# Optimization experiments

Hardware: AMD Instinct MI355X
Metric: run time of the kernel (lower is better)

Reference implementation:

```python
import jax, jax.numpy as jnp
import numpy as np

HS = 128  # hidden_size
B, L = 2, 1024


def setup_inputs() -> dict:
    key = jax.random.key(0)
    k = jax.random.split(key, 3)
    d = HS
    X = jax.random.normal(k[0], (B, L, d), dtype=jnp.float32)
    # mlp: Linear(4d -> d), GELU, Linear(d -> 1)
    W1 = jax.random.normal(k[1], (4 * d, d), dtype=jnp.float32) / np.sqrt(4 * d).astype(np.float32)
    b1 = jnp.zeros((d,), dtype=jnp.float32)
    W2 = jax.random.normal(k[2], (d, 1), dtype=jnp.float32) / np.sqrt(d).astype(np.float32)
    b2 = jnp.zeros((1,), dtype=jnp.float32)
    return {"X": X, "W1": W1, "b1": b1, "W2": W2, "b2": b2}


def reference(X, W1, b1, W2, b2):
    # f = cat([Xi, Xj, Xi-Xj, Xi*Xj]) @ W1  decomposes exactly into four matmuls:
    #   Xi@(Wi+Wd) + Xj@(Wj-Wd) + (Xi*Xj)@Wp
    # avoiding the (b,l,l,4d) concat tensor.
    b, l, d = X.shape
    Wi, Wj, Wd, Wp = jnp.split(W1, 4, axis=0)  # each (d, h)
    A = X @ (Wi + Wd)                           # (b,l,h): depends on i only
    Bm = X @ (Wj - Wd)                          # (b,l,h): depends on j only
    P = jnp.einsum('bid,bjd,dh->bijh', X, X, Wp)  # elementwise-product term
    h = jax.nn.gelu(A[:, :, None, :] + Bm[:, None, :, :] + P + b1,
                    approximate=False)          # (b,l,l,h), exact GELU like nn.GELU()
    out = jnp.einsum('bijh,ho->bij', h, W2) + b2[0]  # (b,l,l)
    out = jax.nn.relu(out)
    out = 0.5 * (out + jnp.swapaxes(out, 1, 2))      # symmetrize
    diag_mask = 1.0 - jnp.eye(l, dtype=out.dtype)    # zero the diagonal
    return out * diag_mask
```

## Files before the change

### kernel.cpp

```cpp
#include <hip/hip_runtime.h>


typedef __attribute__((ext_vector_type(8))) short short8;
typedef __attribute__((ext_vector_type(16))) float f32x16;
typedef __attribute__((ext_vector_type(2))) float f32x2;

#define NT 32
#define NTRI 528
#define IPB 16

__device__ __forceinline__ unsigned short f2bf(float f) {
  unsigned int u = __float_as_uint(f);
  u = (u + 0x7fffu + ((u >> 16) & 1u)) >> 16;
  return (unsigned short)u;
}

__device__ __forceinline__ short8 pack8(float4 a, float4 b) {
  short8 r;
  r[0] = (short)f2bf(a.x); r[1] = (short)f2bf(a.y);
  r[2] = (short)f2bf(a.z); r[3] = (short)f2bf(a.w);
  r[4] = (short)f2bf(b.x); r[5] = (short)f2bf(b.y);
  r[6] = (short)f2bf(b.z); r[7] = (short)f2bf(b.w);
  return r;
}

__device__ __forceinline__ f32x2 gelu_2(f32x2 x) {
  f32x2 t = x * x;
  f32x2 u = x * __builtin_elementwise_fma(t, (f32x2)0.10295205f, (f32x2)2.30220725f);
  f32x2 e;
  e[0] = __builtin_amdgcn_exp2f(u[0]);
  e[1] = __builtin_amdgcn_exp2f(u[1]);
  f32x2 ep = e + 1.0f;
  f32x2 r;
  r[0] = __builtin_amdgcn_rcpf(ep[0]);
  r[1] = __builtin_amdgcn_rcpf(ep[1]);
  return __builtin_elementwise_fma(-x, r, x);
}

__global__ void k0_prep_w(const float* __restrict__ W1, unsigned short* __restrict__ wsT) {
  int idx = blockIdx.x * 256 + threadIdx.x;
  int arr = idx >> 14, rem = idx & 16383, h = rem >> 7, d = rem & 127;
  float v;
  if (arr == 0)      v = W1[d * 128 + h] + W1[(256 + d) * 128 + h];
  else if (arr == 1) v = W1[(128 + d) * 128 + h] - W1[(256 + d) * 128 + h];
  else               v = W1[(384 + d) * 128 + h];
  wsT[idx] = f2bf(v);
}

__global__ __launch_bounds__(256) void k1_ab(const float* __restrict__ X,
                                             const unsigned short* __restrict__ wsT,
                                             const float* __restrict__ b1,
                                             float* __restrict__ Aout,
                                             float* __restrict__ Bout) {
  int tid = threadIdx.x, w = tid >> 6, lane = tid & 63, jl = lane & 31, hi = lane >> 5;
  int row0 = blockIdx.x * 64;
  int c0 = w * 64;
  f32x16 a00 = (f32x16)0.f, a01 = (f32x16)0.f, a10 = (f32x16)0.f, a11 = (f32x16)0.f;
#pragma unroll
  for (int s = 0; s < 8; ++s) {
    const float* xp0 = X + (size_t)(row0 + jl) * 128 + s * 16 + hi * 8;
    const float* xp1 = xp0 + 32 * 128;
    short8 fa0 = pack8(*(const float4*)xp0, *(const float4*)(xp0 + 4));
    short8 fa1 = pack8(*(const float4*)xp1, *(const float4*)(xp1 + 4));
    short8 fb0 = *(const short8*)(wsT + (size_t)(c0 + jl) * 128 + s * 16 + hi * 8);
    short8 fb1 = *(const short8*)(wsT + (size_t)(c0 + 32 + jl) * 128 + s * 16 + hi * 8);
    a00 = __builtin_amdgcn_mfma_f32_32x32x16_bf16(fa0, fb0, a00, 0, 0, 0);
    a01 = __builtin_amdgcn_mfma_f32_32x32x16_bf16(fa0, fb1, a01, 0, 0, 0);
    a10 = __builtin_amdgcn_mfma_f32_32x32x16_bf16(fa1, fb0, a10, 0, 0, 0);
    a11 = __builtin_amdgcn_mfma_f32_32x32x16_bf16(fa1, fb1, a11, 0, 0, 0);
  }
  bool isB = (c0 >= 128);
  float b1v0 = 0.f, b1v1 = 0.f;
  if (isB) { b1v0 = b1[c0 - 128 + jl]; b1v1 = b1[c0 - 96 + jl]; }
#pragma unroll
  for (int q = 0; q < 16; ++q) {
    int r = (q & 3) + 8 * (q >> 2) + 4 * hi;
    int bl0 = row0 + r, bl1 = row0 + 32 + r;
    if (!isB) {
      Aout[(size_t)bl0 * 128 + c0 + jl]      = a00[q];
      Aout[(size_t)bl0 * 128 + c0 + 32 + jl] = a01[q];
      Aout[(size_t)bl1 * 128 + c0 + jl]      = a10[q];
      Aout[(size_t)bl1 * 128 + c0 + 32 + jl] = a11[q];
    } else {
      Bout[(size_t)bl0 * 128 + c0 - 128 + jl] = a00[q] + b1v0;
      Bout[(size_t)bl0 * 128 + c0 - 96 + jl]  = a01[q] + b1v1;
      Bout[(size_t)bl1 * 128 + c0 - 128 + jl] = a10[q] + b1v0;
      Bout[(size_t)bl1 * 128 + c0 - 96 + jl]  = a11[q] + b1v1;
    }
  }
}

union BfPack { __bf16 h[16]; short8 v[2]; };

__global__ __launch_bounds__(256) void k2_main(const float* __restrict__ X,
                                               const unsigned short* __restrict__ WpT,
                                               const float* __restrict__ Aws,
                                               const float* __restrict__ Bws,
                                               const float* __restrict__ W2,
                                               const float* __restrict__ b2,
                                               float* __restrict__ out) {
  __shared__ __align__(16) unsigned short Mlds[2][32 * 128];
  __shared__ __align__(16) float Abias[IPB][128];
  __shared__ __align__(16) float Bbias[IPB][128];
  __shared__ __align__(16) float W2l[128];
  __shared__ float2 osum[2][4][32];
  __shared__ float valbuf[IPB][33];

  int bid = blockIdx.x;
  int half = bid & 1;
  int tl = bid >> 1;
  int b = tl / NTRI;
  int t = tl - b * NTRI;
  int ti = 0;
  while (t >= NT - ti) { t -= NT - ti; ++ti; }
  int tj = ti + t;
  int gi0 = ti * 32, gj0 = tj * 32;
  int giBase = gi0 + half * IPB;

  int tid = threadIdx.x, w = tid >> 6, lane = tid & 63, jl = lane & 31, hi = lane >> 5;
  int dseg = tid >> 5;
  int gj = gj0 + jl;
  const size_t rowX = (size_t)b * 1024;

  float xj[16], bmj[16], ajv[16];
  {
    const float* xjp = X + (rowX + gj0 + jl) * 128 + dseg * 16;
    *(float4*)(xj + 0)  = *(const float4*)(xjp + 0);
    *(float4*)(xj + 4)  = *(const float4*)(xjp + 4);
    *(float4*)(xj + 8)  = *(const float4*)(xjp + 8);
    *(float4*)(xj + 12) = *(const float4*)(xjp + 12);
  }
#pragma unroll
  for (int g = 0; g < 4; ++g) {
    int hb = 8 * g + 4 * hi + 32 * w;
    *(float4*)(bmj + 4 * g) = *(const float4*)(Bws + (rowX + gj) * 128 + hb);
    *(float4*)(ajv + 4 * g) = *(const float4*)(Aws + (rowX + gj) * 128 + hb);
  }
  short8 afrag[8];
#pragma unroll
  for (int s = 0; s < 8; ++s)
    afrag[s] = *(const short8*)(WpT + (size_t)(w * 32 + jl) * 128 + s * 16 + hi * 8);
  float b2s = b2[0];

  char* mB0 = (char*)Mlds[0];
  char* mB1 = (char*)Mlds[1];
  int rbase = jl * 256;
  int swz = (jl & 15) << 4;

  {
    int r = tid >> 4, c = (tid & 15) * 8;
    const float* ap = Aws + (rowX + giBase + r) * 128 + c;
    const float* bp = Bws + (rowX + giBase + r) * 128 + c;
    *(float4*)(&Abias[r][c])     = *(const float4*)(ap);
    *(float4*)(&Abias[r][c + 4]) = *(const float4*)(ap + 4);
    *(float4*)(&Bbias[r][c])     = *(const float4*)(bp);
    *(float4*)(&Bbias[r][c + 4]) = *(const float4*)(bp + 4);
    if (tid < 128) W2l[tid] = W2[tid];
  }

  auto loadXrow = [&](int gi, float* xv) {
    const float* xip = X + (rowX + gi) * 128 + dseg * 16;
    *(float4*)(xv + 0)  = *(const float4*)(xip + 0);
    *(float4*)(xv + 4)  = *(const float4*)(xip + 4);
    *(float4*)(xv + 8)  = *(const float4*)(xip + 8);
    *(float4*)(xv + 12) = *(const float4*)(xip + 12);
  };
  auto writeM = [&](const float* xv, char* mp) {
    BfPack mb;
#pragma unroll
    for (int r = 0; r < 8; ++r) {
      f32x2 xa = { xv[2 * r], xv[2 * r + 1] };
      f32x2 xb = { xj[2 * r], xj[2 * r + 1] };
      f32x2 pr = xa * xb;
      mb.h[2 * r]     = (__bf16)pr[0];
      mb.h[2 * r + 1] = (__bf16)pr[1];
    }
    *(short8*)(mp + rbase + ((dseg * 32 + 0) ^ swz))  = mb.v[0];
    *(short8*)(mp + rbase + ((dseg * 32 + 16) ^ swz)) = mb.v[1];
  };
  auto mfmaTile = [&](const char* mr) -> f32x16 {
    f32x16 acc = (f32x16)0.0f;
#pragma unroll
    for (int s = 0; s < 8; ++s) {
      short8 bf = *(const short8*)(mr + rbase + (((2 * s + hi) * 16) ^ swz));
      acc = __builtin_amdgcn_mfma_f32_32x32x16_bf16(afrag[s], bf, acc, 0, 0, 0);
    }
    return acc;
  };
  auto finalize = [&](int r, int slot) {
    int j = (w << 3) + lane;
    float2 p0 = osum[slot][0][j], p1 = osum[slot][1][j];
    float2 p2 = osum[slot][2][j], p3 = osum[slot][3][j];
    float s1 = p0.x + p1.x + p2.x + p3.x + b2s;
    float s2 = p0.y + p1.y + p2.y + p3.y + b2s;
    float v = 0.5f * (fmaxf(s1, 0.f) + fmaxf(s2, 0.f));
    int gi = giBase + r;
    if (ti == tj && gj0 + j == gi) v = 0.f;
    out[(rowX + gi) * 1024 + gj0 + j] = v;
    valbuf[r][j] = v;
  };

  {
    float xv0[16];
    loadXrow(giBase + 0, xv0);
    writeM(xv0, mB0);
  }
  __syncthreads();

#pragma unroll 2
  for (int i = 0; i < IPB; ++i) {
    float xvN[16];
    if (i + 1 < IPB) loadXrow(giBase + i + 1, xvN);
    float aiv[16], biv[16], w2h[16];
#pragma unroll
    for (int g = 0; g < 4; ++g) {
      int hb = 8 * g + 4 * hi + 32 * w;
      *(float4*)(aiv + 4 * g) = *(const float4*)(&Abias[i][hb]);
      *(float4*)(biv + 4 * g) = *(const float4*)(&Bbias[i][hb]);
      *(float4*)(w2h + 4 * g) = *(const float4*)(&W2l[hb]);
    }
    f32x16 acc = mfmaTile((i & 1) ? mB1 : mB0);
    if (i >= 1 && lane < 8) finalize(i - 1, (i - 1) & 1);
    {
      f32x2 o1v = { 0.f, 0.f }, o2v = { 0.f, 0.f };
#pragma unroll
      for (int k = 0; k < 8; ++k) {
        f32x2 p   = { acc[2 * k], acc[2 * k + 1] };
        f32x2 a_i = { aiv[2 * k], aiv[2 * k + 1] };
        f32x2 b_i = { biv[2 * k], biv[2 * k + 1] };
        f32x2 a_j = { ajv[2 * k], ajv[2 * k + 1] };
        f32x2 b_j = { bmj[2 * k], bmj[2 * k + 1] };
        f32x2 wv  = { w2h[2 * k], w2h[2 * k + 1] };
        f32x2 g1 = gelu_2((p + a_i) + b_j);
        f32x2 g2 = gelu_2((p + a_j) + b_i);
        o1v = __builtin_elementwise_fma(g1, wv, o1v);
        o2v = __builtin_elementwise_fma(g2, wv, o2v);
      }
      float o1 = o1v[0] + o1v[1], o2 = o2v[0] + o2v[1];
      o1 += __shfl_xor(o1, 32);
      o2 += __shfl_xor(o2, 32);
      if (lane < 32) { osum[i & 1][w][lane] = make_float2(o1, o2); }
    }
    if (i + 1 < IPB) writeM(xvN, ((i + 1) & 1) ? mB1 : mB0);
    __syncthreads();
  }

  if (lane < 8) finalize(IPB - 1, (IPB - 1) & 1);
  __syncthreads();

  if (ti != tj && tid < 128) {
    int j = tid >> 2, i0 = (tid & 3) * 4;
    float4 v;
    v.x = valbuf[i0 + 0][j]; v.y = valbuf[i0 + 1][j];
    v.z = valbuf[i0 + 2][j]; v.w = valbuf[i0 + 3][j];
    *(float4*)(out + (rowX + gj0 + j) * 1024 + giBase + i0) = v;
  }
}

extern "C" void kernel_launch(void* const* d_in, const int* in_sizes, int n_in,
                              void* d_out, int out_size, void* d_ws, size_t ws_size,
                              hipStream_t stream) {
  (void)in_sizes; (void)n_in; (void)out_size; (void)ws_size;
  const float* X  = (const float*)d_in[0];
  const float* W1 = (const float*)d_in[1];
  const float* b1 = (const float*)d_in[2];
  const float* W2 = (const float*)d_in[3];
  const float* b2 = (const float*)d_in[4];
  float* out = (float*)d_out;

  unsigned short* wsT = (unsigned short*)d_ws;
  unsigned short* WpT = wsT + 2 * 16384;
  float* Aws = (float*)((char*)d_ws + 98304);
  float* Bws = (float*)((char*)d_ws + 98304 + 1048576);

  k0_prep_w<<<192, 256, 0, stream>>>(W1, wsT);
  k1_ab<<<32, 256, 0, stream>>>(X, wsT, b1, Aws, Bws);
  k2_main<<<4 * NTRI, 256, 0, stream>>>(X, WpT, Aws, Bws, W2, b2, out);
}
```

Measured before the change: 146.5 us.

## Software-pipeline MFMA and GELU epilogue across row pairs with quad-buffered LDS

Restructures the main loop to handle two i-rows per iteration. The MFMA tiles for the current pair are issued while the GELU epilogue runs on the previous pair's accumulators, and the X-product tiles for the next pair are built at the same time. LDS grows to four M buffers and osum gains a slot dimension, which halves the number of block barriers. The cost is more registers for the held accumulators and extra LDS, which may reduce occupancy.

Result: slower. 195.2 us (+33.3%).

```diff
diff --git a/kernel.cpp b/kernel.cpp
--- a/kernel.cpp
+++ b/kernel.cpp
@@ -99,11 +99,11 @@
                                                const float* __restrict__ W2,
                                                const float* __restrict__ b2,
                                                float* __restrict__ out) {
-  __shared__ __align__(16) unsigned short Mlds[2][32 * 128];
+  __shared__ __align__(16) unsigned short Mlds[4][32 * 128];
   __shared__ __align__(16) float Abias[IPB][128];
   __shared__ __align__(16) float Bbias[IPB][128];
   __shared__ __align__(16) float W2l[128];
-  __shared__ float2 osum[2][4][32];
+  __shared__ float2 osum[2][2][4][32];
   __shared__ float valbuf[IPB][33];
 
   int bid = blockIdx.x;
@@ -142,8 +142,6 @@
     afrag[s] = *(const short8*)(WpT + (size_t)(w * 32 + jl) * 128 + s * 16 + hi * 8);
   float b2s = b2[0];
 
-  char* mB0 = (char*)Mlds[0];
-  char* mB1 = (char*)Mlds[1];
   int rbase = jl * 256;
   int swz = (jl & 15) << 4;
 
@@ -187,10 +185,38 @@
     }
     return acc;
   };
-  auto finalize = [&](int r, int slot) {
+  auto epilogue = [&](const f32x16& acc, int r, int par, int sl) {
+    float aiv[16], biv[16], w2h[16];
+#pragma unroll
+    for (int g = 0; g < 4; ++g) {
+      int hb = 8 * g + 4 * hi + 32 * w;
+      *(float4*)(aiv + 4 * g) = *(const float4*)(&Abias[r][hb]);
+      *(float4*)(biv + 4 * g) = *(const float4*)(&Bbias[r][hb]);
+      *(float4*)(w2h + 4 * g) = *(const float4*)(&W2l[hb]);
+    }
+    f32x2 o1v = { 0.f, 0.f }, o2v = { 0.f, 0.f };
+#pragma unroll
+    for (int k = 0; k < 8; ++k) {
+      f32x2 p   = { acc[2 * k], acc[2 * k + 1] };
+      f32x2 a_i = { aiv[2 * k], aiv[2 * k + 1] };
+      f32x2 b_i = { biv[2 * k], biv[2 * k + 1] };
+      f32x2 a_j = { ajv[2 * k], ajv[2 * k + 1] };
+      f32x2 b_j = { bmj[2 * k], bmj[2 * k + 1] };
+      f32x2 wv  = { w2h[2 * k], w2h[2 * k + 1] };
+      f32x2 g1 = gelu_2((p + a_i) + b_j);
+      f32x2 g2 = gelu_2((p + a_j) + b_i);
+      o1v = __builtin_elementwise_fma(g1, wv, o1v);
+      o2v = __builtin_elementwise_fma(g2, wv, o2v);
+    }
+    float o1 = o1v[0] + o1v[1], o2 = o2v[0] + o2v[1];
+    o1 += __shfl_xor(o1, 32);
+    o2 += __shfl_xor(o2, 32);
+    if (lane < 32) { osum[par][sl][w][lane] = make_float2(o1, o2); }
+  };
+  auto finalize = [&](int r, int par, int sl) {
     int j = (w << 3) + lane;
-    float2 p0 = osum[slot][0][j], p1 = osum[slot][1][j];
-    float2 p2 = osum[slot][2][j], p3 = osum[slot][3][j];
+    float2 p0 = osum[par][sl][0][j], p1 = osum[par][sl][1][j];
+    float2 p2 = osum[par][sl][2][j], p3 = osum[par][sl][3][j];
     float s1 = p0.x + p1.x + p2.x + p3.x + b2s;
     float s2 = p0.y + p1.y + p2.y + p3.y + b2s;
     float v = 0.5f * (fmaxf(s1, 0.f) + fmaxf(s2, 0.f));
@@ -201,51 +227,52 @@
   };
 
   {
-    float xv0[16];
+    float xv0[16], xv1[16];
     loadXrow(giBase + 0, xv0);
-    writeM(xv0, mB0);
+    loadXrow(giBase + 1, xv1);
+    writeM(xv0, (char*)Mlds[0]);
+    writeM(xv1, (char*)Mlds[1]);
   }
   __syncthreads();
 
-#pragma unroll 2
-  for (int i = 0; i < IPB; ++i) {
-    float xvN[16];
-    if (i + 1 < IPB) loadXrow(giBase + i + 1, xvN);
-    float aiv[16], biv[16], w2h[16];
-#pragma unroll
-    for (int g = 0; g < 4; ++g) {
-      int hb = 8 * g + 4 * hi + 32 * w;
-      *(float4*)(aiv + 4 * g) = *(const float4*)(&Abias[i][hb]);
-      *(float4*)(biv + 4 * g) = *(const float4*)(&Bbias[i][hb]);
-      *(float4*)(w2h + 4 * g) = *(const float4*)(&W2l[hb]);
-    }
-    f32x16 acc = mfmaTile((i & 1) ? mB1 : mB0);
-    if (i >= 1 && lane < 8) finalize(i - 1, (i - 1) & 1);
-    {
-      f32x2 o1v = { 0.f, 0.f }, o2v = { 0.f, 0.f };
-#pragma unroll
-      for (int k = 0; k < 8; ++k) {
-        f32x2 p   = { acc[2 * k], acc[2 * k + 1] };
-        f32x2 a_i = { aiv[2 * k], aiv[2 * k + 1] };
-        f32x2 b_i = { biv[2 * k], biv[2 * k + 1] };
-        f32x2 a_j = { ajv[2 * k], ajv[2 * k + 1] };
-        f32x2 b_j = { bmj[2 * k], bmj[2 * k + 1] };
-        f32x2 wv  = { w2h[2 * k], w2h[2 * k + 1] };
-        f32x2 g1 = gelu_2((p + a_i) + b_j);
-        f32x2 g2 = gelu_2((p + a_j) + b_i);
-        o1v = __builtin_elementwise_fma(g1, wv, o1v);
-        o2v = __builtin_elementwise_fma(g2, wv, o2v);
-      }
-      float o1 = o1v[0] + o1v[1], o2 = o2v[0] + o2v[1];
-      o1 += __shfl_xor(o1, 32);
-      o2 += __shfl_xor(o2, 32);
-      if (lane < 32) { osum[i & 1][w][lane] = make_float2(o1, o2); }
-    }
-    if (i + 1 < IPB) writeM(xvN, ((i + 1) & 1) ? mB1 : mB0);
+  f32x16 pA = (f32x16)0.f, pB = (f32x16)0.f;
+
+#pragma unroll 3
+  for (int p = 0; p <= 8; ++p) {
+    if (p >= 2 && lane < 8) {
+      finalize(2 * (p - 2),     (p - 2) & 1, 0);
+      finalize(2 * (p - 2) + 1, (p - 2) & 1, 1);
+    }
+    float xvA[16], xvB[16];
+    bool doBuild = (2 * p + 2 < IPB);
+    if (doBuild) {
+      loadXrow(giBase + 2 * p + 2, xvA);
+      loadXrow(giBase + 2 * p + 3, xvB);
+    }
+    f32x16 nA, nB;
+    bool doMfma = (p < 8);
+    if (doMfma) {
+      const char* m0 = (const char*)Mlds[(p & 1) * 2 + 0];
+      const char* m1 = (const char*)Mlds[(p & 1) * 2 + 1];
+      nA = mfmaTile(m0);
+      nB = mfmaTile(m1);
+    }
+    if (p >= 1) {
+      epilogue(pA, 2 * (p - 1),     (p - 1) & 1, 0);
+      epilogue(pB, 2 * (p - 1) + 1, (p - 1) & 1, 1);
+    }
+    if (doBuild) {
+      writeM(xvA, (char*)Mlds[((p + 1) & 1) * 2 + 0]);
+      writeM(xvB, (char*)Mlds[((p + 1) & 1) * 2 + 1]);
+    }
+    if (doMfma) { pA = nA; pB = nB; }
     __syncthreads();
   }
 
-  if (lane < 8) finalize(IPB - 1, (IPB - 1) & 1);
+  if (lane < 8) {
+    finalize(IPB - 2, 7 & 1, 0);
+    finalize(IPB - 1, 7 & 1, 1);
+  }
   __syncthreads();
 
   if (ti != tj && tid < 128) {
```

## Build MFMA B-operand in registers and drop per-row LDS double buffer and barriers

Applied to the files above, without the earlier changes.

Each thread now holds 64 floats of its X_j row and forms the bf16 X_i*X_j fragments directly in registers from an LDS copy of the 16 X_i rows, instead of cooperatively writing a swizzled bf16 product tile to double-buffered LDS every row. This removes one __syncthreads per row. The per-row finalize is deferred to a single block-wide pass over an enlarged osum buffer. It also removes the software pipelining of X loads and raises register pressure (xjr[64]), and each wave now does the product and convert work redundantly. That may lower occupancy or add VALU work.

New measurement: 149.7 us. 2.2% more time.

```diff
diff --git a/kernel.cpp b/kernel.cpp
--- a/kernel.cpp
+++ b/kernel.cpp
@@ -90,7 +90,7 @@
   }
 }
 
-union BfPack { __bf16 h[16]; short8 v[2]; };
+union Bf8 { __bf16 h[8]; short8 v; };
 
 __global__ __launch_bounds__(256) void k2_main(const float* __restrict__ X,
                                                const unsigned short* __restrict__ WpT,
@@ -99,11 +99,11 @@
                                                const float* __restrict__ W2,
                                                const float* __restrict__ b2,
                                                float* __restrict__ out) {
-  __shared__ __align__(16) unsigned short Mlds[2][32 * 128];
+  __shared__ __align__(16) float Xp[IPB][128];
   __shared__ __align__(16) float Abias[IPB][128];
   __shared__ __align__(16) float Bbias[IPB][128];
   __shared__ __align__(16) float W2l[128];
-  __shared__ float2 osum[2][4][32];
+  __shared__ float2 osum[IPB][4][32];
   __shared__ float valbuf[IPB][33];
 
   int bid = blockIdx.x;
@@ -118,39 +118,16 @@
   int giBase = gi0 + half * IPB;
 
   int tid = threadIdx.x, w = tid >> 6, lane = tid & 63, jl = lane & 31, hi = lane >> 5;
-  int dseg = tid >> 5;
+  const size_t rowX = (size_t)b * 1024;
   int gj = gj0 + jl;
-  const size_t rowX = (size_t)b * 1024;
-
-  float xj[16], bmj[16], ajv[16];
-  {
-    const float* xjp = X + (rowX + gj0 + jl) * 128 + dseg * 16;
-    *(float4*)(xj + 0)  = *(const float4*)(xjp + 0);
-    *(float4*)(xj + 4)  = *(const float4*)(xjp + 4);
-    *(float4*)(xj + 8)  = *(const float4*)(xjp + 8);
-    *(float4*)(xj + 12) = *(const float4*)(xjp + 12);
-  }
-#pragma unroll
-  for (int g = 0; g < 4; ++g) {
-    int hb = 8 * g + 4 * hi + 32 * w;
-    *(float4*)(bmj + 4 * g) = *(const float4*)(Bws + (rowX + gj) * 128 + hb);
-    *(float4*)(ajv + 4 * g) = *(const float4*)(Aws + (rowX + gj) * 128 + hb);
-  }
-  short8 afrag[8];
-#pragma unroll
-  for (int s = 0; s < 8; ++s)
-    afrag[s] = *(const short8*)(WpT + (size_t)(w * 32 + jl) * 128 + s * 16 + hi * 8);
-  float b2s = b2[0];
-
-  char* mB0 = (char*)Mlds[0];
-  char* mB1 = (char*)Mlds[1];
-  int rbase = jl * 256;
-  int swz = (jl & 15) << 4;
 
   {
     int r = tid >> 4, c = (tid & 15) * 8;
+    const float* xp = X   + (rowX + giBase + r) * 128 + c;
     const float* ap = Aws + (rowX + giBase + r) * 128 + c;
     const float* bp = Bws + (rowX + giBase + r) * 128 + c;
+    *(float4*)(&Xp[r][c])        = *(const float4*)(xp);
+    *(float4*)(&Xp[r][c + 4])    = *(const float4*)(xp + 4);
     *(float4*)(&Abias[r][c])     = *(const float4*)(ap);
     *(float4*)(&Abias[r][c + 4]) = *(const float4*)(ap + 4);
     *(float4*)(&Bbias[r][c])     = *(const float4*)(bp);
@@ -158,94 +135,84 @@
     if (tid < 128) W2l[tid] = W2[tid];
   }
 
-  auto loadXrow = [&](int gi, float* xv) {
-    const float* xip = X + (rowX + gi) * 128 + dseg * 16;
-    *(float4*)(xv + 0)  = *(const float4*)(xip + 0);
-    *(float4*)(xv + 4)  = *(const float4*)(xip + 4);
-    *(float4*)(xv + 8)  = *(const float4*)(xip + 8);
-    *(float4*)(xv + 12) = *(const float4*)(xip + 12);
-  };
-  auto writeM = [&](const float* xv, char* mp) {
-    BfPack mb;
-#pragma unroll
-    for (int r = 0; r < 8; ++r) {
-      f32x2 xa = { xv[2 * r], xv[2 * r + 1] };
-      f32x2 xb = { xj[2 * r], xj[2 * r + 1] };
-      f32x2 pr = xa * xb;
-      mb.h[2 * r]     = (__bf16)pr[0];
-      mb.h[2 * r + 1] = (__bf16)pr[1];
+  float xjr[64];
+#pragma unroll
+  for (int s = 0; s < 8; ++s) {
+    const float* xjp = X + (rowX + gj) * 128 + s * 16 + hi * 8;
+    *(float4*)(xjr + s * 8)     = *(const float4*)(xjp);
+    *(float4*)(xjr + s * 8 + 4) = *(const float4*)(xjp + 4);
+  }
+  float bmj[16], ajv[16];
+#pragma unroll
+  for (int g = 0; g < 4; ++g) {
+    int hb = 8 * g + 4 * hi + 32 * w;
+    *(float4*)(bmj + 4 * g) = *(const float4*)(Bws + (rowX + gj) * 128 + hb);
+    *(float4*)(ajv + 4 * g) = *(const float4*)(Aws + (rowX + gj) * 128 + hb);
+  }
+  short8 afrag[8];
+#pragma unroll
+  for (int s = 0; s < 8; ++s)
+    afrag[s] = *(const short8*)(WpT + (size_t)(w * 32 + jl) * 128 + s * 16 + hi * 8);
+  float b2s = b2[0];
+
+  __syncthreads();
+
+#pragma unroll 1
+  for (int i = 0; i < IPB; ++i) {
+    f32x16 acc = (f32x16)0.0f;
+#pragma unroll
+    for (int s = 0; s < 8; ++s) {
+      const float* xip = &Xp[i][s * 16 + hi * 8];
+      float4 xi0 = *(const float4*)(xip);
+      float4 xi1 = *(const float4*)(xip + 4);
+      Bf8 mb;
+      mb.h[0] = (__bf16)(xi0.x * xjr[s * 8 + 0]);
+      mb.h[1] = (__bf16)(xi0.y * xjr[s * 8 + 1]);
+      mb.h[2] = (__bf16)(xi0.z * xjr[s * 8 + 2]);
+      mb.h[3] = (__bf16)(xi0.w * xjr[s * 8 + 3]);
+      mb.h[4] = (__bf16)(xi1.x * xjr[s * 8 + 4]);
+      mb.h[5] = (__bf16)(xi1.y * xjr[s * 8 + 5]);
+      mb.h[6] = (__bf16)(xi1.z * xjr[s * 8 + 6]);
+      mb.h[7] = (__bf16)(xi1.w * xjr[s * 8 + 7]);
+      acc = __builtin_amdgcn_mfma_f32_32x32x16_bf16(afrag[s], mb.v, acc, 0, 0, 0);
     }
-    *(short8*)(mp + rbase + ((dseg * 32 + 0) ^ swz))  = mb.v[0];
-    *(short8*)(mp + rbase + ((dseg * 32 + 16) ^ swz)) = mb.v[1];
-  };
-  auto mfmaTile = [&](const char* mr) -> f32x16 {
-    f32x16 acc = (f32x16)0.0f;
-#pragma unroll
-    for (int s = 0; s < 8; ++s) {
-      short8 bf = *(const short8*)(mr + rbase + (((2 * s + hi) * 16) ^ swz));
-      acc = __builtin_amdgcn_mfma_f32_32x32x16_bf16(afrag[s], bf, acc, 0, 0, 0);
+    f32x2 o1v = { 0.f, 0.f }, o2v = { 0.f, 0.f };
+#pragma unroll
+    for (int k = 0; k < 8; ++k) {
+      int hb = ((2 * k) & 3) + 8 * ((2 * k) >> 2) + 4 * hi + 32 * w;
+      f32x2 aiv = *(const f32x2*)(&Abias[i][hb]);
+      f32x2 biv = *(const f32x2*)(&Bbias[i][hb]);
+      f32x2 wv  = *(const f32x2*)(&W2l[hb]);
+      f32x2 p   = { acc[2 * k], acc[2 * k + 1] };
+      f32x2 b_j = { bmj[2 * k], bmj[2 * k + 1] };
+      f32x2 a_j = { ajv[2 * k], ajv[2 * k + 1] };
+      f32x2 g1 = gelu_2((p + aiv) + b_j);
+      f32x2 g2 = gelu_2((p + a_j) + biv);
+      o1v = __builtin_elementwise_fma(g1, wv, o1v);
+      o2v = __builtin_elementwise_fma(g2, wv, o2v);
     }
-    return acc;
-  };
-  auto finalize = [&](int r, int slot) {
-    int j = (w << 3) + lane;
-    float2 p0 = osum[slot][0][j], p1 = osum[slot][1][j];
-    float2 p2 = osum[slot][2][j], p3 = osum[slot][3][j];
+    float o1 = o1v[0] + o1v[1], o2 = o2v[0] + o2v[1];
+    o1 += __shfl_xor(o1, 32);
+    o2 += __shfl_xor(o2, 32);
+    if (lane < 32) osum[i][w][lane] = make_float2(o1, o2);
+  }
+
+  __syncthreads();
+
+#pragma unroll
+  for (int pass = 0; pass < 2; ++pass) {
+    int i = (tid >> 5) + pass * 8;
+    int j = tid & 31;
+    float2 p0 = osum[i][0][j], p1 = osum[i][1][j];
+    float2 p2 = osum[i][2][j], p3 = osum[i][3][j];
     float s1 = p0.x + p1.x + p2.x + p3.x + b2s;
     float s2 = p0.y + p1.y + p2.y + p3.y + b2s;
     float v = 0.5f * (fmaxf(s1, 0.f) + fmaxf(s2, 0.f));
-    int gi = giBase + r;
+    int gi = giBase + i;
     if (ti == tj && gj0 + j == gi) v = 0.f;
     out[(rowX + gi) * 1024 + gj0 + j] = v;
-    valbuf[r][j] = v;
-  };
-
-  {
-    float xv0[16];
-    loadXrow(giBase + 0, xv0);
-    writeM(xv0, mB0);
-  }
-  __syncthreads();
-
-#pragma unroll 2
-  for (int i = 0; i < IPB; ++i) {
-    float xvN[16];
-    if (i + 1 < IPB) loadXrow(giBase + i + 1, xvN);
-    float aiv[16], biv[16], w2h[16];
-#pragma unroll
-    for (int g = 0; g < 4; ++g) {
-      int hb = 8 * g + 4 * hi + 32 * w;
-      *(float4*)(aiv + 4 * g) = *(const float4*)(&Abias[i][hb]);
-      *(float4*)(biv + 4 * g) = *(const float4*)(&Bbias[i][hb]);
-      *(float4*)(w2h + 4 * g) = *(const float4*)(&W2l[hb]);
-    }
-    f32x16 acc = mfmaTile((i & 1) ? mB1 : mB0);
-    if (i >= 1 && lane < 8) finalize(i - 1, (i - 1) & 1);
-    {
-      f32x2 o1v = { 0.f, 0.f }, o2v = { 0.f, 0.f };
-#pragma unroll
-      for (int k = 0; k < 8; ++k) {
-        f32x2 p   = { acc[2 * k], acc[2 * k + 1] };
-        f32x2 a_i = { aiv[2 * k], aiv[2 * k + 1] };
-        f32x2 b_i = { biv[2 * k], biv[2 * k + 1] };
-        f32x2 a_j = { ajv[2 * k], ajv[2 * k + 1] };
-        f32x2 b_j = { bmj[2 * k], bmj[2 * k + 1] };
-        f32x2 wv  = { w2h[2 * k], w2h[2 * k + 1] };
-        f32x2 g1 = gelu_2((p + a_i) + b_j);
-        f32x2 g2 = gelu_2((p + a_j) + b_i);
-        o1v = __builtin_elementwise_fma(g1, wv, o1v);
-        o2v = __builtin_elementwise_fma(g2, wv, o2v);
-      }
-      float o1 = o1v[0] + o1v[1], o2 = o2v[0] + o2v[1];
-      o1 += __shfl_xor(o1, 32);
-      o2 += __shfl_xor(o2, 32);
-      if (lane < 32) { osum[i & 1][w][lane] = make_float2(o1, o2); }
-    }
-    if (i + 1 < IPB) writeM(xvN, ((i + 1) & 1) ? mB1 : mB0);
-    __syncthreads();
-  }
-
-  if (lane < 8) finalize(IPB - 1, (IPB - 1) & 1);
+    valbuf[i][j] = v;
+  }
   __syncthreads();
 
   if (ti != tj && tid < 128) {
```

## Software-pipeline MFMA with previous row's GELU epilogue and stage X rows in LDS

Applied to the files above, without the earlier changes.

Restructures the per-row loop so the MFMA for row i is issued while the GELU/W2 epilogue for row i-1 runs, giving the matrix unit and the vector ALUs independent work to overlap. Finalization is delayed by two rows to match. X rows for the block are now staged into LDS up front instead of being loaded from global memory each iteration. Bias and W2 values are read from LDS inside the epilogue as float2 pairs rather than preloaded into registers. This keeps an extra 16-float accumulator live across iterations, which raises register pressure, and the loop is no longer unrolled.

Result: faster. 139.3 us (-4.9%).

```diff
diff --git a/kernel.cpp b/kernel.cpp
--- a/kernel.cpp
+++ b/kernel.cpp
@@ -100,6 +100,7 @@
                                                const float* __restrict__ b2,
                                                float* __restrict__ out) {
   __shared__ __align__(16) unsigned short Mlds[2][32 * 128];
+  __shared__ __align__(16) float Xp[IPB][128];
   __shared__ __align__(16) float Abias[IPB][128];
   __shared__ __align__(16) float Bbias[IPB][128];
   __shared__ __align__(16) float W2l[128];
@@ -122,35 +123,13 @@
   int gj = gj0 + jl;
   const size_t rowX = (size_t)b * 1024;
 
-  float xj[16], bmj[16], ajv[16];
-  {
-    const float* xjp = X + (rowX + gj0 + jl) * 128 + dseg * 16;
-    *(float4*)(xj + 0)  = *(const float4*)(xjp + 0);
-    *(float4*)(xj + 4)  = *(const float4*)(xjp + 4);
-    *(float4*)(xj + 8)  = *(const float4*)(xjp + 8);
-    *(float4*)(xj + 12) = *(const float4*)(xjp + 12);
-  }
-#pragma unroll
-  for (int g = 0; g < 4; ++g) {
-    int hb = 8 * g + 4 * hi + 32 * w;
-    *(float4*)(bmj + 4 * g) = *(const float4*)(Bws + (rowX + gj) * 128 + hb);
-    *(float4*)(ajv + 4 * g) = *(const float4*)(Aws + (rowX + gj) * 128 + hb);
-  }
-  short8 afrag[8];
-#pragma unroll
-  for (int s = 0; s < 8; ++s)
-    afrag[s] = *(const short8*)(WpT + (size_t)(w * 32 + jl) * 128 + s * 16 + hi * 8);
-  float b2s = b2[0];
-
-  char* mB0 = (char*)Mlds[0];
-  char* mB1 = (char*)Mlds[1];
-  int rbase = jl * 256;
-  int swz = (jl & 15) << 4;
-
   {
     int r = tid >> 4, c = (tid & 15) * 8;
+    const float* xp = X   + (rowX + giBase + r) * 128 + c;
     const float* ap = Aws + (rowX + giBase + r) * 128 + c;
     const float* bp = Bws + (rowX + giBase + r) * 128 + c;
+    *(float4*)(&Xp[r][c])        = *(const float4*)(xp);
+    *(float4*)(&Xp[r][c + 4])    = *(const float4*)(xp + 4);
     *(float4*)(&Abias[r][c])     = *(const float4*)(ap);
     *(float4*)(&Abias[r][c + 4]) = *(const float4*)(ap + 4);
     *(float4*)(&Bbias[r][c])     = *(const float4*)(bp);
@@ -158,14 +137,38 @@
     if (tid < 128) W2l[tid] = W2[tid];
   }
 
-  auto loadXrow = [&](int gi, float* xv) {
-    const float* xip = X + (rowX + gi) * 128 + dseg * 16;
+  float xj[16], bmj[16], ajv[16];
+  {
+    const float* xjp = X + (rowX + gj) * 128 + dseg * 16;
+    *(float4*)(xj + 0)  = *(const float4*)(xjp + 0);
+    *(float4*)(xj + 4)  = *(const float4*)(xjp + 4);
+    *(float4*)(xj + 8)  = *(const float4*)(xjp + 8);
+    *(float4*)(xj + 12) = *(const float4*)(xjp + 12);
+  }
+#pragma unroll
+  for (int g = 0; g < 4; ++g) {
+    int hb = 8 * g + 4 * hi + 32 * w;
+    *(float4*)(bmj + 4 * g) = *(const float4*)(Bws + (rowX + gj) * 128 + hb);
+    *(float4*)(ajv + 4 * g) = *(const float4*)(Aws + (rowX + gj) * 128 + hb);
+  }
+  short8 afrag[8];
+#pragma unroll
+  for (int s = 0; s < 8; ++s)
+    afrag[s] = *(const short8*)(WpT + (size_t)(w * 32 + jl) * 128 + s * 16 + hi * 8);
+  float b2s = b2[0];
+
+  char* mB0 = (char*)Mlds[0];
+  char* mB1 = (char*)Mlds[1];
+  int rbase = jl * 256;
+  int swz = (jl & 15) << 4;
+
+  auto writeM = [&](int i, char* mp) {
+    const float* xip = &Xp[i][dseg * 16];
+    float xv[16];
     *(float4*)(xv + 0)  = *(const float4*)(xip + 0);
     *(float4*)(xv + 4)  = *(const float4*)(xip + 4);
     *(float4*)(xv + 8)  = *(const float4*)(xip + 8);
     *(float4*)(xv + 12) = *(const float4*)(xip + 12);
-  };
-  auto writeM = [&](const float* xv, char* mp) {
     BfPack mb;
 #pragma unroll
     for (int r = 0; r < 8; ++r) {
@@ -187,8 +190,30 @@
     }
     return acc;
   };
-  auto finalize = [&](int r, int slot) {
+  auto epilogue = [&](const f32x16& acc, int r) {
+    f32x2 o1v = { 0.f, 0.f }, o2v = { 0.f, 0.f };
+#pragma unroll
+    for (int k = 0; k < 8; ++k) {
+      int hb = ((2 * k) & 3) + 8 * ((2 * k) >> 2) + 4 * hi + 32 * w;
+      f32x2 aiv = *(const f32x2*)(&Abias[r][hb]);
+      f32x2 biv = *(const f32x2*)(&Bbias[r][hb]);
+      f32x2 wv  = *(const f32x2*)(&W2l[hb]);
+      f32x2 p   = { acc[2 * k], acc[2 * k + 1] };
+      f32x2 b_j = { bmj[2 * k], bmj[2 * k + 1] };
+      f32x2 a_j = { ajv[2 * k], ajv[2 * k + 1] };
+      f32x2 g1 = gelu_2((p + aiv) + b_j);
+      f32x2 g2 = gelu_2((p + a_j) + biv);
+      o1v = __builtin_elementwise_fma(g1, wv, o1v);
+      o2v = __builtin_elementwise_fma(g2, wv, o2v);
+    }
+    float o1 = o1v[0] + o1v[1], o2 = o2v[0] + o2v[1];
+    o1 += __shfl_xor(o1, 32);
+    o2 += __shfl_xor(o2, 32);
+    if (lane < 32) osum[r & 1][w][lane] = make_float2(o1, o2);
+  };
+  auto finalize = [&](int r) {
     int j = (w << 3) + lane;
+    int slot = r & 1;
     float2 p0 = osum[slot][0][j], p1 = osum[slot][1][j];
     float2 p2 = osum[slot][2][j], p3 = osum[slot][3][j];
     float s1 = p0.x + p1.x + p2.x + p3.x + b2s;
@@ -200,52 +225,26 @@
     valbuf[r][j] = v;
   };
 
-  {
-    float xv0[16];
-    loadXrow(giBase + 0, xv0);
-    writeM(xv0, mB0);
-  }
-  __syncthreads();
-
-#pragma unroll 2
+  __syncthreads();
+  writeM(0, mB0);
+  __syncthreads();
+
+  f32x16 accP;
+
+#pragma unroll 1
   for (int i = 0; i < IPB; ++i) {
-    float xvN[16];
-    if (i + 1 < IPB) loadXrow(giBase + i + 1, xvN);
-    float aiv[16], biv[16], w2h[16];
-#pragma unroll
-    for (int g = 0; g < 4; ++g) {
-      int hb = 8 * g + 4 * hi + 32 * w;
-      *(float4*)(aiv + 4 * g) = *(const float4*)(&Abias[i][hb]);
-      *(float4*)(biv + 4 * g) = *(const float4*)(&Bbias[i][hb]);
-      *(float4*)(w2h + 4 * g) = *(const float4*)(&W2l[hb]);
-    }
-    f32x16 acc = mfmaTile((i & 1) ? mB1 : mB0);
-    if (i >= 1 && lane < 8) finalize(i - 1, (i - 1) & 1);
-    {
-      f32x2 o1v = { 0.f, 0.f }, o2v = { 0.f, 0.f };
-#pragma unroll
-      for (int k = 0; k < 8; ++k) {
-        f32x2 p   = { acc[2 * k], acc[2 * k + 1] };
-        f32x2 a_i = { aiv[2 * k], aiv[2 * k + 1] };
-        f32x2 b_i = { biv[2 * k], biv[2 * k + 1] };
-        f32x2 a_j = { ajv[2 * k], ajv[2 * k + 1] };
-        f32x2 b_j = { bmj[2 * k], bmj[2 * k + 1] };
-        f32x2 wv  = { w2h[2 * k], w2h[2 * k + 1] };
-        f32x2 g1 = gelu_2((p + a_i) + b_j);
-        f32x2 g2 = gelu_2((p + a_j) + b_i);
-        o1v = __builtin_elementwise_fma(g1, wv, o1v);
-        o2v = __builtin_elementwise_fma(g2, wv, o2v);
-      }
-      float o1 = o1v[0] + o1v[1], o2 = o2v[0] + o2v[1];
-      o1 += __shfl_xor(o1, 32);
-      o2 += __shfl_xor(o2, 32);
-      if (lane < 32) { osum[i & 1][w][lane] = make_float2(o1, o2); }
-    }
-    if (i + 1 < IPB) writeM(xvN, ((i + 1) & 1) ? mB1 : mB0);
+    if (i >= 2 && lane < 8) finalize(i - 2);
+    f32x16 accC = mfmaTile((i & 1) ? mB1 : mB0);
+    if (i >= 1) epilogue(accP, i - 1);
+    if (i + 1 < IPB) writeM(i + 1, ((i + 1) & 1) ? mB1 : mB0);
+    accP = accC;
     __syncthreads();
   }
 
-  if (lane < 8) finalize(IPB - 1, (IPB - 1) & 1);
+  if (lane < 8) finalize(IPB - 2);
+  epilogue(accP, IPB - 1);
+  __syncthreads();
+  if (lane < 8) finalize(IPB - 1);
   __syncthreads();
 
   if (ti != tj && tid < 128) {
```
